# Optimization experiments

Hardware: AMD Instinct MI355X
Metric: run time of the kernel (lower is better)

Reference implementation:

```python
import jax, jax.numpy as jnp
import numpy as np

NEG_FILL = -1e20
SPANS_PER_WORD = 2


def setup_inputs() -> dict:
    key = jax.random.key(0)
    k1, k2, k3, k4, k5 = jax.random.split(key, 5)
    B, N, D, T = 8, 16384, 256, 8
    embeddings = jax.random.normal(k1, (B, N, D), dtype=jnp.float32)
    scores_a = jax.random.normal(k2, (B, N, T), dtype=jnp.float32)
    scores_b = jax.random.normal(k3, (B, N, T), dtype=jnp.float32)
    span_mask = jax.random.randint(k4, (B, N), 0, 2).astype(bool)
    seq_length = jax.random.randint(k5, (B,), 1, 2048).astype(jnp.int32)
    return {
        "embeddings": embeddings,
        "scores_a": scores_a,
        "scores_b": scores_b,
        "span_mask": span_mask,
        "seq_length": seq_length,
    }


def reference(embeddings, scores_a, scores_b, span_mask, seq_length):
    # --- SpanPruner.forward: per-dict-entry softmax, drop null tag, max over tags ---
    probs_list = [jnp.max(jax.nn.softmax(s, axis=2)[:, :, 1:], axis=2)
                  for s in (scores_a, scores_b)]
    probabilities = jnp.maximum(probs_list[0], probs_list[1])  # max over dict entries  [B,N]

    # --- span_pruner ---
    num_keep = jnp.maximum(seq_length * SPANS_PER_WORD, 1)       # [B]
    max_keep = int(jnp.max(num_keep))                            # static k for topk

    scores = jnp.where(span_mask, probabilities, NEG_FILL)       # masked_fill  [B,N]
    _, top_indices = jax.lax.top_k(scores, max_keep)             # [B,K], descending like torch.topk

    top_indices_mask = jnp.arange(max_keep)[None, :] < num_keep[:, None]  # [B,K]
    fill_value = jnp.max(top_indices, axis=1, keepdims=True)
    top_indices = jnp.where(top_indices_mask, top_indices, fill_value)
    top_indices = jnp.sort(top_indices, axis=1)                  # [B,K]

    # batched_index_select gathers
    seq_mask = jnp.take_along_axis(span_mask, top_indices, axis=1)        # [B,K] bool
    top_mask = (top_indices_mask & seq_mask).astype(jnp.int32)            # [B,K]
    top_scores = jnp.take_along_axis(scores, top_indices, axis=1)         # [B,K]
    top_embeddings = jnp.take_along_axis(embeddings, top_indices[:, :, None], axis=1)  # [B,K,D]

    return top_indices, top_embeddings, top_scores, top_mask
```

## Files before the change

### kernel.cpp

```cpp
#include <hip/hip_runtime.h>
#include <math.h>

#define NB 8
#define NN 16384
#define NT 8
#define ND 256
#define NEG_FILL_F (-1e20f)

__device__ __forceinline__ unsigned fkey(float s){
  unsigned u = __float_as_uint(s);
  return (u & 0x80000000u) ? ~u : (u | 0x80000000u);
}
__device__ __forceinline__ float fkey_inv(unsigned k){
  unsigned u = (k & 0x80000000u) ? (k ^ 0x80000000u) : ~k;
  return __uint_as_float(u);
}

__device__ __forceinline__ float prob_of(const float4 x, const float4 y){
  float m = fmaxf(fmaxf(fmaxf(x.x,x.y),fmaxf(x.z,x.w)),
                  fmaxf(fmaxf(y.x,y.y),fmaxf(y.z,y.w)));
  float e0=expf(x.x-m), e1=expf(x.y-m), e2=expf(x.z-m), e3=expf(x.w-m);
  float e4=expf(y.x-m), e5=expf(y.y-m), e6=expf(y.z-m), e7=expf(y.w-m);
  float sum = ((((((e0+e1)+e2)+e3)+e4)+e5)+e6)+e7;
  float pm = fmaxf(fmaxf(fmaxf(e1,e2),fmaxf(e3,e4)),fmaxf(fmaxf(e5,e6),e7));
  return pm/sum;
}

__global__ void k_scores(const float* __restrict__ sa, const float* __restrict__ sb,
                         const int* __restrict__ mask, unsigned* __restrict__ outk){
  int i = blockIdx.x*blockDim.x + threadIdx.x;
  if (i >= NB*NN) return;
  const float4* pa = (const float4*)(sa + (size_t)i*NT);
  const float4* pb = (const float4*)(sb + (size_t)i*NT);
  float4 a0=pa[0], a1=pa[1], b0=pb[0], b1=pb[1];
  float p = fmaxf(prob_of(a0,a1), prob_of(b0,b1));
  outk[i] = fkey(mask[i] ? p : NEG_FILL_F);
}

__device__ int block_scan_excl(int v, int* lds, int tid){
  __syncthreads();
  int lane = tid & 63, wave = tid >> 6;
  int x = v;
  #pragma unroll
  for (int off=1; off<64; off<<=1){
    int y = __shfl_up(x, off, 64);
    if (lane >= off) x += y;
  }
  if (lane == 63) lds[wave] = x;
  __syncthreads();
  if (wave == 0){
    int w = (lane < 16) ? lds[lane] : 0;
    #pragma unroll
    for (int off=1; off<16; off<<=1){
      int y = __shfl_up(w, off, 64);
      if (lane >= off) w += y;
    }
    if (lane < 16) lds[16+lane] = w;
  }
  __syncthreads();
  int waveOff = wave ? lds[16+wave-1] : 0;
  return waveOff + x - v;
}

__global__ __launch_bounds__(1024)
void k_select(const unsigned* __restrict__ keys, const int* __restrict__ seq,
              float* __restrict__ out, int K){
  const int b = blockIdx.x;
  const int tid = threadIdx.x;
  const int lane = tid & 63, wave = tid >> 6;
  __shared__ unsigned whist[16][257];
  __shared__ int hist[256];
  __shared__ int P[256];
  __shared__ int lds[32];
  __shared__ int lds4[4];
  __shared__ int smax[16];
  __shared__ int sBin, sRem, sFill;

  int num_keep = seq[b]*2; if (num_keep < 1) num_keep = 1;

  const unsigned* kb = keys + (size_t)b*NN + tid*16;
  unsigned kk[16];
  #pragma unroll
  for (int q=0;q<4;++q){
    uint4 v = ((const uint4*)kb)[q];
    kk[4*q+0]=v.x; kk[4*q+1]=v.y; kk[4*q+2]=v.z; kk[4*q+3]=v.w;
  }

  unsigned TK=0, TN=0; int needK=0, needN=0;
  for (int sel=0; sel<2; ++sel){
    int r = sel ? num_keep : K;
    unsigned pref=0, decided=0;
    for (int round=0; round<4; ++round){
      const int shift = 24 - 8*round;
      #pragma unroll
      for (int i=0;i<4;++i) whist[wave][lane + 64*i] = 0u;
      __syncthreads();
      #pragma unroll
      for (int j=0;j<16;++j){
        unsigned k = kk[j];
        if (((k ^ pref) & decided) == 0u)
          atomicAdd(&whist[wave][(k>>shift)&255u], 1u);
      }
      __syncthreads();
      if (tid < 256){
        unsigned sum=0;
        #pragma unroll
        for (int w=0;w<16;++w) sum += whist[w][tid];
        hist[tid] = (int)sum;
      }
      __syncthreads();
      int Pt = 0;
      if (tid < 256){
        int x = hist[255 - tid];
        #pragma unroll
        for (int off=1; off<64; off<<=1){
          int y = __shfl_up(x, off, 64);
          if (lane >= off) x += y;
        }
        if (lane==63) lds4[wave] = x;
        Pt = x;
      }
      __syncthreads();
      if (tid < 256){
        int offs = 0;
        for (int w=0; w<wave; ++w) offs += lds4[w];
        Pt += offs;
        P[tid] = Pt;
      }
      __syncthreads();
      if (tid < 256){
        int prev = (tid==0) ? 0 : P[tid-1];
        if (Pt >= r && prev < r){
          sBin = 255 - tid;
          sRem = r - prev;
        }
      }
      __syncthreads();
      pref |= ((unsigned)sBin) << shift;
      r = sRem;
      decided |= (0xFFu << shift);
      __syncthreads();
    }
    if (sel){ TN=pref; needN=r; } else { TK=pref; needK=r; }
  }

  int cTK=0, cTN=0;
  #pragma unroll
  for (int j=0;j<16;++j){
    unsigned k = kk[j];
    cTK += (k==TK); cTN += (k==TN);
  }
  int oTK = block_scan_excl(cTK, lds, tid);
  int oTN = block_scan_excl(cTN, lds, tid);

  const int base = tid*16;
  int tK=oTK, tN=oTN, cKept=0, maxIdx=-1;
  #pragma unroll
  for (int j=0;j<16;++j){
    unsigned k=kk[j];
    bool inK  = (k>TK) || ((k==TK) && (tK<needK));  if (k==TK) tK++;
    bool kept = (k>TN) || ((k==TN) && (tN<needN));  if (k==TN) tN++;
    if (inK) maxIdx = base+j;
    cKept += kept;
  }
  int oKept = block_scan_excl(cKept, lds, tid);

  int mv=maxIdx;
  #pragma unroll
  for (int off=32; off; off>>=1){
    int y = __shfl_down(mv, off, 64);
    mv = mv > y ? mv : y;
  }
  if (lane==0) smax[wave]=mv;
  __syncthreads();
  if (tid==0){
    int f=-1;
    for (int i=0;i<16;++i) f = f > smax[i] ? f : smax[i];
    sFill = f;
  }
  __syncthreads();
  const int fill = sFill;

  float* out_idx = out;
  float* out_sc  = out + (size_t)NB*K + (size_t)NB*K*ND;
  float* out_mk  = out_sc + (size_t)NB*K;
  const int ob = b*K;
  const unsigned kNEG = fkey(NEG_FILL_F);

  int tN2=oTN, p=oKept;
  #pragma unroll
  for (int j=0;j<16;++j){
    unsigned k=kk[j];
    bool kept = (k>TN) || ((k==TN) && (tN2<needN));  if (k==TN) tN2++;
    if (kept){
      int n = base+j;
      out_idx[ob+p] = (float)n;
      out_sc[ob+p]  = fkey_inv(k);
      out_mk[ob+p]  = (k != kNEG) ? 1.0f : 0.0f;
      ++p;
    }
  }
  if (num_keep < K){
    float fs = fkey_inv(keys[(size_t)b*NN + fill]);
    for (int q = num_keep + tid; q < K; q += 1024){
      out_idx[ob+q] = (float)fill;
      out_sc[ob+q]  = fs;
      out_mk[ob+q]  = 0.0f;
    }
  }
}

__global__ void k_gather(const float* __restrict__ emb, const float* __restrict__ out_idx,
                         float* __restrict__ out_emb, int K){
  size_t g = (size_t)blockIdx.x*blockDim.x + threadIdx.x;
  size_t total = (size_t)NB*K*(ND/4);
  if (g >= total) return;
  int c = (int)(g & (ND/4 - 1));
  size_t r = g >> 6;
  int bK = (int)r;
  int b = bK / K;
  int idx = (int)out_idx[r];
  const float4* src = (const float4*)(emb + ((size_t)b*NN + (size_t)idx)*ND);
  float4* dst = (float4*)(out_emb + r*(size_t)ND);
  dst[c] = src[c];
}

extern "C" void kernel_launch(void* const* d_in, const int* in_sizes, int n_in,
                              void* d_out, int out_size, void* d_ws, size_t ws_size,
                              hipStream_t stream) {
  const float* emb  = (const float*)d_in[0];
  const float* sa   = (const float*)d_in[1];
  const float* sb   = (const float*)d_in[2];
  const int*   mask = (const int*)d_in[3];
  const int*   seq  = (const int*)d_in[4];
  float* out = (float*)d_out;
  unsigned* ws_keys = (unsigned*)d_ws;

  int K = out_size / (NB*(ND+3));
  if (K <= 0) return;

  k_scores<<<(NB*NN + 255)/256, 256, 0, stream>>>(sa, sb, mask, ws_keys);
  k_select<<<NB, 1024, 0, stream>>>(ws_keys, seq, out, K);
  size_t total = (size_t)NB*K*(ND/4);
  k_gather<<<(int)((total + 255)/256), 256, 0, stream>>>(emb, out, out + (size_t)NB*K, K);
}
```

Measured before the change: 222.2 us.

## Build first radix-select histogram in scores kernel and share rounds between selections

The scores kernel now builds a per-batch histogram of the top key byte, using shared-memory atomics followed by global atomics, so the select kernel skips its first histogram round. The two radix selections (K and num_keep) now share histogram rounds while their prefixes match, and a separate pass runs only once they diverge. This cuts the number of barrier-heavy rounds in the single-block-per-batch select kernel. In exchange it adds a zeroing kernel launch and global atomics in the scores kernel.

```diff
diff --git a/kernel.cpp b/kernel.cpp
--- a/kernel.cpp
+++ b/kernel.cpp
@@ -26,15 +26,30 @@
   return pm/sum;
 }
 
+__global__ void k_zero(int* __restrict__ ghist){
+  int i = blockIdx.x*blockDim.x + threadIdx.x;
+  if (i < NB*256) ghist[i] = 0;
+}
+
 __global__ void k_scores(const float* __restrict__ sa, const float* __restrict__ sb,
-                         const int* __restrict__ mask, unsigned* __restrict__ outk){
-  int i = blockIdx.x*blockDim.x + threadIdx.x;
-  if (i >= NB*NN) return;
+                         const int* __restrict__ mask, unsigned* __restrict__ outk,
+                         int* __restrict__ ghist){
+  __shared__ int lh[256];
+  const int t = threadIdx.x;
+  lh[t] = 0;
+  __syncthreads();
+  int i = blockIdx.x*256 + t;
   const float4* pa = (const float4*)(sa + (size_t)i*NT);
   const float4* pb = (const float4*)(sb + (size_t)i*NT);
   float4 a0=pa[0], a1=pa[1], b0=pb[0], b1=pb[1];
   float p = fmaxf(prob_of(a0,a1), prob_of(b0,b1));
-  outk[i] = fkey(mask[i] ? p : NEG_FILL_F);
+  unsigned k = fkey(mask[i] ? p : NEG_FILL_F);
+  outk[i] = k;
+  atomicAdd(&lh[k>>24], 1);
+  __syncthreads();
+  int b = blockIdx.x >> 6;
+  int v = lh[t];
+  if (v) atomicAdd(&ghist[b*256 + t], v);
 }
 
 __device__ int block_scan_excl(int v, int* lds, int tid){
@@ -62,9 +77,58 @@
   return waveOff + x - v;
 }
 
+__device__ void build_hist(const unsigned* kk, unsigned pref, unsigned decided, int shift,
+                           unsigned (*whist)[257], int* hist, int tid, int lane, int wave){
+  #pragma unroll
+  for (int i=0;i<4;++i) whist[wave][lane + 64*i] = 0u;
+  __syncthreads();
+  #pragma unroll
+  for (int j=0;j<16;++j){
+    unsigned k = kk[j];
+    if (((k ^ pref) & decided) == 0u)
+      atomicAdd(&whist[wave][(k>>shift)&255u], 1u);
+  }
+  __syncthreads();
+  if (tid < 256){
+    unsigned sum=0;
+    #pragma unroll
+    for (int w=0;w<16;++w) sum += whist[w][tid];
+    hist[tid] = (int)sum;
+  }
+  __syncthreads();
+}
+
+__device__ void scan_pick2(int x, int r0, int r1, bool do1,
+                           int* P, int* lds4, int* sOut, int tid, int lane, int wave){
+  int Pt = 0;
+  if (tid < 256){
+    #pragma unroll
+    for (int off=1; off<64; off<<=1){
+      int y = __shfl_up(x, off, 64);
+      if (lane >= off) x += y;
+    }
+    if (lane==63) lds4[wave] = x;
+    Pt = x;
+  }
+  __syncthreads();
+  if (tid < 256){
+    int offs = 0;
+    for (int w=0; w<wave; ++w) offs += lds4[w];
+    Pt += offs;
+    P[tid] = Pt;
+  }
+  __syncthreads();
+  if (tid < 256){
+    int prev = tid ? P[tid-1] : 0;
+    if (Pt >= r0 && prev < r0){ sOut[0] = 255-tid; sOut[1] = r0-prev; }
+    if (do1 && Pt >= r1 && prev < r1){ sOut[2] = 255-tid; sOut[3] = r1-prev; }
+  }
+  __syncthreads();
+}
+
 __global__ __launch_bounds__(1024)
-void k_select(const unsigned* __restrict__ keys, const int* __restrict__ seq,
-              float* __restrict__ out, int K){
+void k_select(const unsigned* __restrict__ keys, const int* __restrict__ ghist,
+              const int* __restrict__ seq, float* __restrict__ out, int K){
   const int b = blockIdx.x;
   const int tid = threadIdx.x;
   const int lane = tid & 63, wave = tid >> 6;
@@ -74,7 +138,8 @@
   __shared__ int lds[32];
   __shared__ int lds4[4];
   __shared__ int smax[16];
-  __shared__ int sBin, sRem, sFill;
+  __shared__ int sOut[4];
+  __shared__ int sFill;
 
   int num_keep = seq[b]*2; if (num_keep < 1) num_keep = 1;
 
@@ -86,63 +151,37 @@
     kk[4*q+0]=v.x; kk[4*q+1]=v.y; kk[4*q+2]=v.z; kk[4*q+3]=v.w;
   }
 
-  unsigned TK=0, TN=0; int needK=0, needN=0;
-  for (int sel=0; sel<2; ++sel){
-    int r = sel ? num_keep : K;
-    unsigned pref=0, decided=0;
-    for (int round=0; round<4; ++round){
-      const int shift = 24 - 8*round;
-      #pragma unroll
-      for (int i=0;i<4;++i) whist[wave][lane + 64*i] = 0u;
+  int r0 = K, r1 = num_keep;
+  int x0 = (tid < 256) ? ghist[b*256 + (255-tid)] : 0;
+  scan_pick2(x0, r0, r1, true, P, lds4, sOut, tid, lane, wave);
+  unsigned pref0 = (unsigned)sOut[0] << 24;  r0 = sOut[1];
+  unsigned pref1 = (unsigned)sOut[2] << 24;  r1 = sOut[3];
+  bool same = (pref0 == pref1);
+  unsigned decided = 0xFF000000u;
+  __syncthreads();
+
+  for (int round=1; round<4; ++round){
+    const int shift = 24 - 8*round;
+    build_hist(kk, pref0, decided, shift, whist, hist, tid, lane, wave);
+    int xv = (tid < 256) ? hist[255-tid] : 0;
+    scan_pick2(xv, r0, r1, same, P, lds4, sOut, tid, lane, wave);
+    int bin0 = sOut[0], rem0 = sOut[1];
+    int bin1 = sOut[2], rem1 = sOut[3];
+    __syncthreads();
+    if (!same){
+      build_hist(kk, pref1, decided, shift, whist, hist, tid, lane, wave);
+      int xv1 = (tid < 256) ? hist[255-tid] : 0;
+      scan_pick2(xv1, r1, 0, false, P, lds4, sOut, tid, lane, wave);
+      bin1 = sOut[0]; rem1 = sOut[1];
       __syncthreads();
-      #pragma unroll
-      for (int j=0;j<16;++j){
-        unsigned k = kk[j];
-        if (((k ^ pref) & decided) == 0u)
-          atomicAdd(&whist[wave][(k>>shift)&255u], 1u);
-      }
-      __syncthreads();
-      if (tid < 256){
-        unsigned sum=0;
-        #pragma unroll
-        for (int w=0;w<16;++w) sum += whist[w][tid];
-        hist[tid] = (int)sum;
-      }
-      __syncthreads();
-      int Pt = 0;
-      if (tid < 256){
-        int x = hist[255 - tid];
-        #pragma unroll
-        for (int off=1; off<64; off<<=1){
-          int y = __shfl_up(x, off, 64);
-          if (lane >= off) x += y;
-        }
-        if (lane==63) lds4[wave] = x;
-        Pt = x;
-      }
-      __syncthreads();
-      if (tid < 256){
-        int offs = 0;
-        for (int w=0; w<wave; ++w) offs += lds4[w];
-        Pt += offs;
-        P[tid] = Pt;
-      }
-      __syncthreads();
-      if (tid < 256){
-        int prev = (tid==0) ? 0 : P[tid-1];
-        if (Pt >= r && prev < r){
-          sBin = 255 - tid;
-          sRem = r - prev;
-        }
-      }
-      __syncthreads();
-      pref |= ((unsigned)sBin) << shift;
-      r = sRem;
-      decided |= (0xFFu << shift);
-      __syncthreads();
-    }
-    if (sel){ TN=pref; needN=r; } else { TK=pref; needK=r; }
-  }
+    }
+    pref0 |= (unsigned)bin0 << shift;  r0 = rem0;
+    pref1 |= (unsigned)bin1 << shift;  r1 = rem1;
+    same = same && (bin0 == bin1);
+    decided |= (0xFFu << shift);
+  }
+  const unsigned TK = pref0;  const int needK = r0;
+  const unsigned TN = pref1;  const int needN = r1;
 
   int cTK=0, cTN=0;
   #pragma unroll
@@ -235,12 +274,14 @@
   const int*   seq  = (const int*)d_in[4];
   float* out = (float*)d_out;
   unsigned* ws_keys = (unsigned*)d_ws;
+  int* ghist = (int*)d_ws + (size_t)NB*NN;
 
   int K = out_size / (NB*(ND+3));
   if (K <= 0) return;
 
-  k_scores<<<(NB*NN + 255)/256, 256, 0, stream>>>(sa, sb, mask, ws_keys);
-  k_select<<<NB, 1024, 0, stream>>>(ws_keys, seq, out, K);
+  k_zero<<<(NB*256 + 255)/256, 256, 0, stream>>>(ghist);
+  k_scores<<<(NB*NN)/256, 256, 0, stream>>>(sa, sb, mask, ws_keys, ghist);
+  k_select<<<NB, 1024, 0, stream>>>(ws_keys, ghist, seq, out, K);
   size_t total = (size_t)NB*K*(ND/4);
   k_gather<<<(int)((total + 255)/256), 256, 0, stream>>>(emb, out, out + (size_t)NB*K, K);
 }
```

Result: faster. 207.4 us (-6.7%).
